# Optimization experiments

Measured on AMD Instinct MI355X. Metric: run time of the kernel, lower is better.

## Reference

```python
import jax, jax.numpy as jnp
import numpy as np
from jax import lax

GAMMA = 0.99
LAM = 0.95
CLIP_PARAM = 0.2
VALUE_LOSS_COEF = 0.5
ENTROPY_COEF = 0.01
EPS = 1e-09

B, T = 4096, 2048


def setup_inputs() -> dict:
    key = jax.random.key(0)
    ks = jax.random.split(key, 6)
    rewards = jax.random.normal(ks[0], (B, T), dtype=jnp.float32)
    values = jax.random.normal(ks[1], (B, T + 1), dtype=jnp.float32)
    ref_probs = jax.random.uniform(ks[2], (B, T), dtype=jnp.float32)
    old_probs = jax.random.uniform(ks[3], (B, T), dtype=jnp.float32)
    curr_probs = jax.random.uniform(ks[4], (B, T), dtype=jnp.float32)
    # episode-continuation masks: mostly 1, occasional 0 (episode boundary)
    masks = (jax.random.uniform(ks[5], (B, T)) > 0.02).astype(jnp.float32)
    return {"rewards": rewards, "values": values, "ref_probs": ref_probs,
            "old_probs": old_probs, "curr_probs": curr_probs, "masks": masks}


def compute_gae(rewards, values, masks, gamma, lam):
    # single fused reverse scan over time; per-step state is (B,)
    def step(carry, xs):
        r, v, v_next, m = xs
        delta = r + gamma * v_next * m - v
        adv = delta + gamma * lam * m * carry
        return adv, adv

    xs = (rewards.T, values[:, :-1].T, values[:, 1:].T, masks.T)  # each (T, B)
    _, advs = lax.scan(step, jnp.zeros(rewards.shape[0], rewards.dtype), xs, reverse=True)
    advantages = advs.T  # (B, T)
    returns = advantages + values[:, :-1]
    return advantages, returns


def reference(rewards, values, ref_probs, old_probs, curr_probs, masks):
    advantages, returns = compute_gae(rewards, values, masks, GAMMA, LAM)
    # torch .std() is unbiased (ddof=1)
    advantages = (advantages - advantages.mean()) / (advantages.std(ddof=1) + EPS)
    ratios = curr_probs / (old_probs + EPS)
    surr1 = ratios * advantages
    surr2 = jnp.clip(ratios, 1.0 - CLIP_PARAM, 1.0 + CLIP_PARAM) * advantages
    ppo_loss = -jnp.minimum(surr1, surr2).mean()
    value_loss = jnp.mean((returns - values[:, :-1]) ** 2)
    entropy_loss = -jnp.mean(curr_probs * jnp.log(curr_probs + EPS))
    total_loss = ppo_loss + VALUE_LOSS_COEF * value_loss + ENTROPY_COEF * entropy_loss
    return (total_loss, ppo_loss, VALUE_LOSS_COEF * value_loss, ENTROPY_COEF * entropy_loss)
```

## Files before the change

### kernel.cpp

```cpp
#include <hip/hip_runtime.h>
#include <math.h>


#define GAMMA     0.99f
#define LAM       0.95f
#define CLIP_LO   0.8f
#define CLIP_HI   1.2f
#define EPSF      1e-9f

constexpr int BB = 4096;
constexpr int TT = 2048;
constexpr long long NN = (long long)BB * TT;
constexpr int GAE_BLOCKS = BB;
constexpr int PPO_BLOCKS = 4096;

struct Stats { float mean; float inv; double sum2; };
static constexpr size_t GAE_PART_OFF = 64;
static constexpr size_t PPO_PART_OFF = GAE_PART_OFF + GAE_BLOCKS * sizeof(float2);
static constexpr size_t ADV_OFF      = PPO_PART_OFF + PPO_BLOCKS * sizeof(float2);

typedef float f32x4 __attribute__((ext_vector_type(4)));

__device__ __forceinline__ unsigned bf16_rne(float x) {
    unsigned u = __float_as_uint(x);
    u += 0x7FFFu + ((u >> 16) & 1u);
    return u >> 16;
}

#define GLOAD(dst, p) \
    asm volatile("global_load_dwordx4 %0, %1, off" : "=v"(dst) : "v"(p))

__global__ __launch_bounds__(256, 4) void gae_kernel(
    const float* __restrict__ rewards,
    const float* __restrict__ values,
    const float* __restrict__ masks,
    uint4* __restrict__ advb,
    float2* __restrict__ partials)
{
    const int tid  = threadIdx.x;
    const int lane = tid & 63;
    const int wave = tid >> 6;
    const int t0   = tid * 8;
    const int r    = blockIdx.x;

    __shared__ float2 wT[4];
    __shared__ float  wr1[4], wr2[4];

    const float* rp = rewards + (size_t)r * TT;
    const float* mp = masks   + (size_t)r * TT;
    const size_t vw = (size_t)r * (TT + 1);
    const int    ofs = (int)(vw & 3);
    const f32x4* v4 = (const f32x4*)(values + (vw & ~(size_t)3));

    f32x4 R0, R1, M0, M1, F0, F1, F2;
    GLOAD(R0, (const f32x4*)(rp + t0));
    GLOAD(R1, (const f32x4*)(rp + t0 + 4));
    GLOAD(M0, (const f32x4*)(mp + t0));
    GLOAD(M1, (const f32x4*)(mp + t0 + 4));
    GLOAD(F0, v4 + 2 * tid);
    GLOAD(F1, v4 + 2 * tid + 1);
    GLOAD(F2, v4 + 2 * tid + 2);
    asm volatile("s_waitcnt vmcnt(0)"
                 : "+v"(R0), "+v"(R1), "+v"(M0), "+v"(M1),
                   "+v"(F0), "+v"(F1), "+v"(F2));
    __builtin_amdgcn_sched_barrier(0);

    float ff[12] = {F0.x, F0.y, F0.z, F0.w, F1.x, F1.y, F1.z, F1.w,
                    F2.x, F2.y, F2.z, F2.w};
    float vv[9];
    if (ofs == 0) {
#pragma unroll
        for (int j = 0; j < 9; ++j) vv[j] = ff[j];
    } else if (ofs == 1) {
#pragma unroll
        for (int j = 0; j < 9; ++j) vv[j] = ff[j + 1];
    } else if (ofs == 2) {
#pragma unroll
        for (int j = 0; j < 9; ++j) vv[j] = ff[j + 2];
    } else {
#pragma unroll
        for (int j = 0; j < 9; ++j) vv[j] = ff[j + 3];
    }

    float rr[8] = {R0.x, R0.y, R0.z, R0.w, R1.x, R1.y, R1.z, R1.w};
    float mm[8] = {M0.x, M0.y, M0.z, M0.w, M1.x, M1.y, M1.z, M1.w};

    float la[8], S[8];
    {
        float d[8], c[8];
#pragma unroll
        for (int j = 0; j < 8; ++j) {
            d[j] = rr[j] + GAMMA * vv[j + 1] * mm[j] - vv[j];
            c[j] = (GAMMA * LAM) * mm[j];
        }
        la[7] = d[7]; S[7] = c[7];
#pragma unroll
        for (int j = 6; j >= 0; --j) {
            la[j] = d[j] + c[j] * la[j + 1];
            S[j]  = c[j] * S[j + 1];
        }
    }

    float A = S[0], Bv = la[0];
#pragma unroll
    for (int d2 = 1; d2 < 64; d2 <<= 1) {
        float A2 = __shfl_down(A, d2, 64), B2 = __shfl_down(Bv, d2, 64);
        if (lane + d2 < 64) { Bv = Bv + A * B2; A = A * A2; }
    }
    if (lane == 0) wT[wave] = make_float2(A, Bv);
    __syncthreads();
    float C = 0.f;
    for (int ww = 3; ww > wave; --ww) C = wT[ww].y + wT[ww].x * C;
    float A1 = __shfl_down(A, 1, 64), B1 = __shfl_down(Bv, 1, 64);
    float car = (lane < 63) ? (B1 + A1 * C) : C;

    float s1 = 0.f, s2 = 0.f;
    unsigned hh[8];
#pragma unroll
    for (int j = 0; j < 8; ++j) {
        float a = la[j] + S[j] * car;
        s1 += a; s2 += a * a;
        hh[j] = bf16_rne(a);
    }
    uint4 pk = {hh[0] | (hh[1] << 16), hh[2] | (hh[3] << 16),
                hh[4] | (hh[5] << 16), hh[6] | (hh[7] << 16)};
    advb[(size_t)r * 256 + tid] = pk;

#pragma unroll
    for (int off = 32; off > 0; off >>= 1) {
        s1 += __shfl_down(s1, off, 64);
        s2 += __shfl_down(s2, off, 64);
    }
    if (lane == 0) { wr1[wave] = s1; wr2[wave] = s2; }
    __syncthreads();
    if (tid == 0) {
        partials[blockIdx.x] = make_float2(wr1[0] + wr1[1] + wr1[2] + wr1[3],
                                           wr2[0] + wr2[1] + wr2[2] + wr2[3]);
    }
}

__global__ __launch_bounds__(256) void finalize_stats(
    const float2* __restrict__ gp, Stats* __restrict__ stats)
{
    const int tid = threadIdx.x;
    __shared__ double l1[256], l2[256];
    double s1 = 0.0, s2 = 0.0;
    for (int i = tid; i < GAE_BLOCKS; i += 256) {
        float2 p = gp[i];
        s1 += (double)p.x;
        s2 += (double)p.y;
    }
    l1[tid] = s1; l2[tid] = s2;
    __syncthreads();
    for (int st = 128; st > 0; st >>= 1) {
        if (tid < st) { l1[tid] += l1[tid + st]; l2[tid] += l2[tid + st]; }
        __syncthreads();
    }
    if (tid == 0) {
        double S1 = l1[0], S2 = l2[0];
        double mean = S1 / (double)NN;
        double var  = (S2 - S1 * S1 / (double)NN) / (double)(NN - 1);
        stats->mean = (float)mean;
        stats->inv  = (float)(1.0 / (sqrt(var) + 1e-9));
        stats->sum2 = S2;
    }
}

__global__ __launch_bounds__(256, 8) void ppo_kernel(
    const float* __restrict__ adv_bf16,
    const float* __restrict__ oldp,
    const float* __restrict__ currp,
    const Stats* __restrict__ stats,
    float2* __restrict__ partials)
{
    const float mean = stats->mean;
    const float inv  = stats->inv;
    const int tid = threadIdx.x;
    const int g   = blockIdx.x * 256 + tid;

    const uint4*  a4 = (const uint4*)adv_bf16;
    const float4* o4 = (const float4*)oldp;
    const float4* c4 = (const float4*)currp;

    uint4  A  = a4[g];
    float4 O0 = o4[2 * g], O1 = o4[2 * g + 1];
    float4 C0 = c4[2 * g], C1 = c4[2 * g + 1];

    float av[8] = {__uint_as_float(A.x << 16), __uint_as_float(A.x & 0xFFFF0000u),
                   __uint_as_float(A.y << 16), __uint_as_float(A.y & 0xFFFF0000u),
                   __uint_as_float(A.z << 16), __uint_as_float(A.z & 0xFFFF0000u),
                   __uint_as_float(A.w << 16), __uint_as_float(A.w & 0xFFFF0000u)};
    float ov[8] = {O0.x, O0.y, O0.z, O0.w, O1.x, O1.y, O1.z, O1.w};
    float cv[8] = {C0.x, C0.y, C0.z, C0.w, C1.x, C1.y, C1.z, C1.w};

    float sm = 0.f, se = 0.f;
#pragma unroll
    for (int j = 0; j < 8; ++j) {
        float an    = (av[j] - mean) * inv;
        float ratio = cv[j] * __builtin_amdgcn_rcpf(ov[j] + EPSF);
        float rc    = fminf(fmaxf(ratio, CLIP_LO), CLIP_HI);
        sm += fminf(ratio * an, rc * an);
        se += cv[j] * __logf(cv[j] + EPSF);
    }

#pragma unroll
    for (int off = 32; off > 0; off >>= 1) {
        sm += __shfl_down(sm, off, 64);
        se += __shfl_down(se, off, 64);
    }
    __shared__ float w1[4], w2[4];
    const int wave = tid >> 6, lane = tid & 63;
    if (lane == 0) { w1[wave] = sm; w2[wave] = se; }
    __syncthreads();
    if (tid == 0) {
        float2 p = {w1[0] + w1[1] + w1[2] + w1[3],
                    w2[0] + w2[1] + w2[2] + w2[3]};
        partials[blockIdx.x] = p;
    }
}

__global__ __launch_bounds__(256) void finalize_out(
    const float2* __restrict__ pp,
    const Stats* __restrict__ stats,
    float* __restrict__ out)
{
    const int tid = threadIdx.x;
    __shared__ double l1[256], l2[256];
    double s1 = 0.0, s2 = 0.0;
    for (int i = tid; i < PPO_BLOCKS; i += 256) {
        float2 p = pp[i];
        s1 += (double)p.x;
        s2 += (double)p.y;
    }
    l1[tid] = s1; l2[tid] = s2;
    __syncthreads();
    for (int st = 128; st > 0; st >>= 1) {
        if (tid < st) { l1[tid] += l1[tid + st]; l2[tid] += l2[tid + st]; }
        __syncthreads();
    }
    if (tid == 0) {
        double invN = 1.0 / (double)NN;
        double vl   = 0.5  * (stats->sum2 * invN);
        double ppo  = -(l1[0] * invN);
        double ent  = -0.01 * (l2[0] * invN);
        out[0] = (float)(ppo + vl + ent);
        out[1] = (float)ppo;
        out[2] = (float)vl;
        out[3] = (float)ent;
    }
}

extern "C" void kernel_launch(void* const* d_in, const int* in_sizes, int n_in,
                              void* d_out, int out_size, void* d_ws, size_t ws_size,
                              hipStream_t stream) {
    const float* rewards = (const float*)d_in[0];
    const float* values  = (const float*)d_in[1];
    const float* oldp    = (const float*)d_in[3];
    const float* currp   = (const float*)d_in[4];
    const float* masks   = (const float*)d_in[5];

    Stats*  stats = (Stats*)d_ws;
    float2* gaep  = (float2*)((char*)d_ws + GAE_PART_OFF);
    float2* ppop  = (float2*)((char*)d_ws + PPO_PART_OFF);
    uint4*  advb  = (uint4*)((char*)d_ws + ADV_OFF);
    float*  out   = (float*)d_out;

    gae_kernel<<<GAE_BLOCKS, 256, 0, stream>>>(rewards, values, masks, advb, gaep);
    finalize_stats<<<1, 256, 0, stream>>>(gaep, stats);
    ppo_kernel<<<PPO_BLOCKS, 256, 0, stream>>>((const float*)advb, oldp, currp, stats, ppop);
    finalize_out<<<1, 256, 0, stream>>>(ppop, stats, out);
}
```

Baseline: 206.8 us.

## Use 512 threads with 4 elements each in GAE and coalesced PPO loads

The GAE kernel now runs 512 threads per row, each handling 4 timesteps instead of 8. This raises parallelism and cuts per-thread registers, and the inline-asm loads are replaced with plain float4 loads. The PPO kernel is restructured so each thread reads two elements 256 apart instead of two adjacent float4s, giving unit-stride coalesced access. The trade-off is a longer cross-wave carry chain (8 waves) and losing the explicit load batching.

```diff
diff --git a/kernel.cpp b/kernel.cpp
--- a/kernel.cpp
+++ b/kernel.cpp
@@ -19,18 +19,13 @@
 static constexpr size_t PPO_PART_OFF = GAE_PART_OFF + GAE_BLOCKS * sizeof(float2);
 static constexpr size_t ADV_OFF      = PPO_PART_OFF + PPO_BLOCKS * sizeof(float2);
 
-typedef float f32x4 __attribute__((ext_vector_type(4)));
-
 __device__ __forceinline__ unsigned bf16_rne(float x) {
     unsigned u = __float_as_uint(x);
     u += 0x7FFFu + ((u >> 16) & 1u);
     return u >> 16;
 }
 
-#define GLOAD(dst, p) \
-    asm volatile("global_load_dwordx4 %0, %1, off" : "=v"(dst) : "v"(p))
-
-__global__ __launch_bounds__(256, 4) void gae_kernel(
+__global__ __launch_bounds__(512, 4) void gae_kernel(
     const float* __restrict__ rewards,
     const float* __restrict__ values,
     const float* __restrict__ masks,
@@ -40,62 +35,53 @@
     const int tid  = threadIdx.x;
     const int lane = tid & 63;
     const int wave = tid >> 6;
-    const int t0   = tid * 8;
+    const int e0   = tid * 4;
     const int r    = blockIdx.x;
 
-    __shared__ float2 wT[4];
-    __shared__ float  wr1[4], wr2[4];
+    __shared__ float2 wT[8];
+    __shared__ float  wr1[8], wr2[8];
 
     const float* rp = rewards + (size_t)r * TT;
     const float* mp = masks   + (size_t)r * TT;
-    const size_t vw = (size_t)r * (TT + 1);
+    const size_t vw  = (size_t)r * (TT + 1);
     const int    ofs = (int)(vw & 3);
-    const f32x4* v4 = (const f32x4*)(values + (vw & ~(size_t)3));
-
-    f32x4 R0, R1, M0, M1, F0, F1, F2;
-    GLOAD(R0, (const f32x4*)(rp + t0));
-    GLOAD(R1, (const f32x4*)(rp + t0 + 4));
-    GLOAD(M0, (const f32x4*)(mp + t0));
-    GLOAD(M1, (const f32x4*)(mp + t0 + 4));
-    GLOAD(F0, v4 + 2 * tid);
-    GLOAD(F1, v4 + 2 * tid + 1);
-    GLOAD(F2, v4 + 2 * tid + 2);
-    asm volatile("s_waitcnt vmcnt(0)"
-                 : "+v"(R0), "+v"(R1), "+v"(M0), "+v"(M1),
-                   "+v"(F0), "+v"(F1), "+v"(F2));
-    __builtin_amdgcn_sched_barrier(0);
-
-    float ff[12] = {F0.x, F0.y, F0.z, F0.w, F1.x, F1.y, F1.z, F1.w,
-                    F2.x, F2.y, F2.z, F2.w};
-    float vv[9];
+    const float4* v4 = (const float4*)(values + (vw & ~(size_t)3));
+
+    float4 R  = *(const float4*)(rp + e0);
+    float4 M  = *(const float4*)(mp + e0);
+    float4 V0 = v4[tid];
+    float4 V1 = v4[tid + 1];
+
+    float ff[8] = {V0.x, V0.y, V0.z, V0.w, V1.x, V1.y, V1.z, V1.w};
+    float vv[5];
     if (ofs == 0) {
 #pragma unroll
-        for (int j = 0; j < 9; ++j) vv[j] = ff[j];
+        for (int j = 0; j < 5; ++j) vv[j] = ff[j];
     } else if (ofs == 1) {
 #pragma unroll
-        for (int j = 0; j < 9; ++j) vv[j] = ff[j + 1];
+        for (int j = 0; j < 5; ++j) vv[j] = ff[j + 1];
     } else if (ofs == 2) {
 #pragma unroll
-        for (int j = 0; j < 9; ++j) vv[j] = ff[j + 2];
+        for (int j = 0; j < 5; ++j) vv[j] = ff[j + 2];
     } else {
 #pragma unroll
-        for (int j = 0; j < 9; ++j) vv[j] = ff[j + 3];
-    }
-
-    float rr[8] = {R0.x, R0.y, R0.z, R0.w, R1.x, R1.y, R1.z, R1.w};
-    float mm[8] = {M0.x, M0.y, M0.z, M0.w, M1.x, M1.y, M1.z, M1.w};
-
-    float la[8], S[8];
+        for (int j = 0; j < 5; ++j) vv[j] = ff[j + 3];
+    }
+
+    float rr[4] = {R.x, R.y, R.z, R.w};
+    float mm[4] = {M.x, M.y, M.z, M.w};
+
+    float la[4], S[4];
     {
-        float d[8], c[8];
-#pragma unroll
-        for (int j = 0; j < 8; ++j) {
+        float d[4], c[4];
+#pragma unroll
+        for (int j = 0; j < 4; ++j) {
             d[j] = rr[j] + GAMMA * vv[j + 1] * mm[j] - vv[j];
             c[j] = (GAMMA * LAM) * mm[j];
         }
-        la[7] = d[7]; S[7] = c[7];
-#pragma unroll
-        for (int j = 6; j >= 0; --j) {
+        la[3] = d[3]; S[3] = c[3];
+#pragma unroll
+        for (int j = 2; j >= 0; --j) {
             la[j] = d[j] + c[j] * la[j + 1];
             S[j]  = c[j] * S[j + 1];
         }
@@ -110,21 +96,20 @@
     if (lane == 0) wT[wave] = make_float2(A, Bv);
     __syncthreads();
     float C = 0.f;
-    for (int ww = 3; ww > wave; --ww) C = wT[ww].y + wT[ww].x * C;
+    for (int ww = 7; ww > wave; --ww) C = wT[ww].y + wT[ww].x * C;
     float A1 = __shfl_down(A, 1, 64), B1 = __shfl_down(Bv, 1, 64);
     float car = (lane < 63) ? (B1 + A1 * C) : C;
 
     float s1 = 0.f, s2 = 0.f;
-    unsigned hh[8];
-#pragma unroll
-    for (int j = 0; j < 8; ++j) {
+    unsigned hh[4];
+#pragma unroll
+    for (int j = 0; j < 4; ++j) {
         float a = la[j] + S[j] * car;
         s1 += a; s2 += a * a;
         hh[j] = bf16_rne(a);
     }
-    uint4 pk = {hh[0] | (hh[1] << 16), hh[2] | (hh[3] << 16),
-                hh[4] | (hh[5] << 16), hh[6] | (hh[7] << 16)};
-    advb[(size_t)r * 256 + tid] = pk;
+    uint2 pk = {hh[0] | (hh[1] << 16), hh[2] | (hh[3] << 16)};
+    ((uint2*)advb)[(size_t)r * 512 + tid] = pk;
 
 #pragma unroll
     for (int off = 32; off > 0; off >>= 1) {
@@ -134,8 +119,10 @@
     if (lane == 0) { wr1[wave] = s1; wr2[wave] = s2; }
     __syncthreads();
     if (tid == 0) {
-        partials[blockIdx.x] = make_float2(wr1[0] + wr1[1] + wr1[2] + wr1[3],
-                                           wr2[0] + wr2[1] + wr2[2] + wr2[3]);
+        float t1 = 0.f, t2 = 0.f;
+#pragma unroll
+        for (int w = 0; w < 8; ++w) { t1 += wr1[w]; t2 += wr2[w]; }
+        partials[blockIdx.x] = make_float2(t1, t2);
     }
 }
 
@@ -176,20 +163,21 @@
     const float mean = stats->mean;
     const float inv  = stats->inv;
     const int tid = threadIdx.x;
-    const int g   = blockIdx.x * 256 + tid;
-
-    const uint4*  a4 = (const uint4*)adv_bf16;
+    const int i0  = blockIdx.x * 512 + tid;
+    const int i1  = i0 + 256;
+
+    const uint2*  a2 = (const uint2*)adv_bf16;
     const float4* o4 = (const float4*)oldp;
     const float4* c4 = (const float4*)currp;
 
-    uint4  A  = a4[g];
-    float4 O0 = o4[2 * g], O1 = o4[2 * g + 1];
-    float4 C0 = c4[2 * g], C1 = c4[2 * g + 1];
-
-    float av[8] = {__uint_as_float(A.x << 16), __uint_as_float(A.x & 0xFFFF0000u),
-                   __uint_as_float(A.y << 16), __uint_as_float(A.y & 0xFFFF0000u),
-                   __uint_as_float(A.z << 16), __uint_as_float(A.z & 0xFFFF0000u),
-                   __uint_as_float(A.w << 16), __uint_as_float(A.w & 0xFFFF0000u)};
+    uint2  A0 = a2[i0], A1 = a2[i1];
+    float4 O0 = o4[i0], O1 = o4[i1];
+    float4 C0 = c4[i0], C1 = c4[i1];
+
+    float av[8] = {__uint_as_float(A0.x << 16), __uint_as_float(A0.x & 0xFFFF0000u),
+                   __uint_as_float(A0.y << 16), __uint_as_float(A0.y & 0xFFFF0000u),
+                   __uint_as_float(A1.x << 16), __uint_as_float(A1.x & 0xFFFF0000u),
+                   __uint_as_float(A1.y << 16), __uint_as_float(A1.y & 0xFFFF0000u)};
     float ov[8] = {O0.x, O0.y, O0.z, O0.w, O1.x, O1.y, O1.z, O1.w};
     float cv[8] = {C0.x, C0.y, C0.z, C0.w, C1.x, C1.y, C1.z, C1.w};
 
@@ -265,7 +253,7 @@
     uint4*  advb  = (uint4*)((char*)d_ws + ADV_OFF);
     float*  out   = (float*)d_out;
 
-    gae_kernel<<<GAE_BLOCKS, 256, 0, stream>>>(rewards, values, masks, advb, gaep);
+    gae_kernel<<<GAE_BLOCKS, 512, 0, stream>>>(rewards, values, masks, advb, gaep);
     finalize_stats<<<1, 256, 0, stream>>>(gaep, stats);
     ppo_kernel<<<PPO_BLOCKS, 256, 0, stream>>>((const float*)advb, oldp, currp, stats, ppop);
     finalize_out<<<1, 256, 0, stream>>>(ppop, stats, out);
```

Result: no change. 207.3 us (+0.2%).
